# Optimization experiments

Hardware: AMD Instinct MI355X
Metric: run time of the kernel (lower is better)

## Reference

```python
import jax, jax.numpy as jnp
import numpy as np
import math

D_MODEL = 1024
NUM_HEADS = 16
HEAD_DIM = D_MODEL // NUM_HEADS
BLOCK_SIZE = 64
THRESHOLD = 0.99


def setup_inputs() -> dict:
    key = jax.random.key(0)
    ks = jax.random.split(key, 12)
    B, S, D = 2, 2048, D_MODEL
    scale = 1.0 / math.sqrt(D)
    x = jax.random.normal(ks[0], (B, S, D), dtype=jnp.float32)
    G_ii = jax.random.uniform(ks[1], (B, S), dtype=jnp.float32)
    # Linear weights stored as [in, out]; applied as x @ W + b (matches nn.Linear math).
    Wq = jax.random.normal(ks[2], (D, D), dtype=jnp.float32) * scale
    bq = jnp.zeros((D,), dtype=jnp.float32)
    Wk = jax.random.normal(ks[3], (D, D), dtype=jnp.float32) * scale
    bk = jnp.zeros((D,), dtype=jnp.float32)
    Wv = jax.random.normal(ks[4], (D, D), dtype=jnp.float32) * scale
    bv = jnp.zeros((D,), dtype=jnp.float32)
    Wo = jax.random.normal(ks[5], (D, D), dtype=jnp.float32) * scale
    bo = jnp.zeros((D,), dtype=jnp.float32)
    return {"x": x, "G_ii": G_ii, "Wq": Wq, "bq": bq, "Wk": Wk, "bk": bk,
            "Wv": Wv, "bv": bv, "Wo": Wo, "bo": bo}


def reference(x, G_ii, Wq, bq, Wk, bk, Wv, bv, Wo, bo):
    B, S, D = x.shape
    H, hd, bs = NUM_HEADS, HEAD_DIM, BLOCK_SIZE
    nb = S // bs

    # Projections and head split: [B, H, S, hd]
    q = (x @ Wq + bq).reshape(B, S, H, hd).transpose(0, 2, 1, 3)
    k = (x @ Wk + bk).reshape(B, S, H, hd).transpose(0, 2, 1, 3)
    v = (x @ Wv + bv).reshape(B, S, H, hd).transpose(0, 2, 1, 3)

    # Per-query-block scattering energy keep mask: block kept iff max |G_ii| >= threshold
    energy = jnp.abs(G_ii)                              # [B, S]
    block_max = energy.reshape(B, nb, bs).max(axis=-1)  # [B, nb]
    keep = (block_max >= THRESHOLD)                     # [B, nb] bool
    row_keep = jnp.repeat(keep, bs, axis=1)             # [B, S]

    # Kept query blocks attend densely (non-causal) over all keys; skipped blocks output zero.
    scores = jnp.einsum('bhqd,bhkd->bhqk', q, k) / math.sqrt(hd)  # [B, H, S, S]
    attn = jax.nn.softmax(scores, axis=-1)
    out = jnp.einsum('bhqk,bhkd->bhqd', attn, v)                  # [B, H, S, hd]
    out = out * row_keep[:, None, :, None].astype(out.dtype)

    out = out.transpose(0, 2, 1, 3).reshape(B, S, D)
    return out @ Wo + bo
```

## Files before the change

### kernel.cpp

```cpp
#include <hip/hip_runtime.h>
#include <math.h>

#define D_MODEL   1024
#define NUM_HEADS 16
#define HEAD_DIM  64
#define BS        64
#define NB        32
#define S_LEN     2048
#define BATCH     2
#define M_ROWS    (BATCH * S_LEN)
#define THRESH    0.99f
#define SCEXP     0.18033688f
#define NPH       (BATCH * NB * NUM_HEADS)
#define SPLITK    4

typedef __attribute__((ext_vector_type(8))) short bf16x8;
typedef __attribute__((ext_vector_type(8))) _Float16 f16x8;
typedef __attribute__((ext_vector_type(2))) __fp16 fp16v2;
typedef __attribute__((ext_vector_type(4))) float f32x4;

__device__ __forceinline__ unsigned short f2bf(float f) {
    unsigned int u = __float_as_uint(f);
    u += 0x7fff + ((u >> 16) & 1);
    return (unsigned short)(u >> 16);
}

__device__ __forceinline__ unsigned int pkrtz(float a, float b) {
    fp16v2 r = __builtin_amdgcn_cvt_pkrtz(a, b);
    return __builtin_bit_cast(unsigned int, r);
}

__device__ __forceinline__ void gload16(const void* gptr, void* lptr) {
    __builtin_amdgcn_global_load_lds(
        (const __attribute__((address_space(1))) void*)gptr,
        (__attribute__((address_space(3))) void*)lptr, 16, 0, 0);
}

__global__ __launch_bounds__(256) void prep_kernel(
    const float* __restrict__ x, const float* __restrict__ G,
    const float* __restrict__ Wq, const float* __restrict__ Wk,
    const float* __restrict__ Wv, const float* __restrict__ Wo,
    unsigned short* __restrict__ xb, unsigned short* __restrict__ wcat,
    unsigned short* __restrict__ wot, int* __restrict__ keep, int* __restrict__ work)
{
    const int bid = blockIdx.x, tid = threadIdx.x;
    __shared__ float T[64][65];

    if (bid < 2048) {
        size_t i = ((size_t)bid * 256 + tid) * 8;
        float4 a = *(const float4*)(x + i);
        float4 b = *(const float4*)(x + i + 4);
        uint4 o;
        o.x = (unsigned int)f2bf(a.x) | ((unsigned int)f2bf(a.y) << 16);
        o.y = (unsigned int)f2bf(a.z) | ((unsigned int)f2bf(a.w) << 16);
        o.z = (unsigned int)f2bf(b.x) | ((unsigned int)f2bf(b.y) << 16);
        o.w = (unsigned int)f2bf(b.z) | ((unsigned int)f2bf(b.w) << 16);
        *(uint4*)(xb + i) = o;
    } else if (bid < 3072) {
        int i = bid - 2048;
        int mat = i >> 8, rem = i & 255;
        int k0 = (rem & 15) * 64, n0 = (rem >> 4) * 64;
        const float* W = (mat == 0) ? Wq : (mat == 1) ? Wk : (mat == 2) ? Wv : Wo;
        int rr = tid >> 4, c4 = (tid & 15) * 4;
        #pragma unroll
        for (int j = 0; j < 4; j++) {
            int row = rr + j * 16;
            float4 v = *(const float4*)(W + (size_t)(k0 + row) * 1024 + n0 + c4);
            T[row][c4 + 0] = v.x; T[row][c4 + 1] = v.y;
            T[row][c4 + 2] = v.z; T[row][c4 + 3] = v.w;
        }
        __syncthreads();
        unsigned short* dst = (mat < 3) ? (wcat + (size_t)mat * 1024 * 1024) : wot;
        #pragma unroll
        for (int j = 0; j < 4; j++) {
            int n = rr + j * 16;
            unsigned int lo = (unsigned int)f2bf(T[c4 + 0][n]) | ((unsigned int)f2bf(T[c4 + 1][n]) << 16);
            unsigned int hi = (unsigned int)f2bf(T[c4 + 2][n]) | ((unsigned int)f2bf(T[c4 + 3][n]) << 16);
            *(uint2*)(dst + (size_t)(n0 + n) * 1024 + k0 + c4) = make_uint2(lo, hi);
        }
    } else {
        if (tid < 64) {
            int t = tid;
            const float4* g = (const float4*)(G + (size_t)t * 64);
            float mx = 0.f;
            #pragma unroll
            for (int j = 0; j < 16; j++) {
                float4 v = g[j];
                mx = fmaxf(mx, fmaxf(fmaxf(fabsf(v.x), fabsf(v.y)), fmaxf(fabsf(v.z), fabsf(v.w))));
            }
            bool k = (mx >= THRESH);
            unsigned long long bal = __ballot(k);
            int nk = __popcll(bal);
            unsigned long long below = bal & ((1ull << t) - 1ull);
            int nbelow = (int)__popcll(below);
            keep[t] = k ? 1 : 0;
            if (t == 0) work[0] = nk;
            int pos = k ? nbelow : (nk + t - nbelow);
            work[1 + pos] = t;
        }
    }
}

__global__ __launch_bounds__(256, 4) void gemm_qkv(
    const unsigned short* __restrict__ A, const unsigned short* __restrict__ Bt,
    const float* __restrict__ bq, const float* __restrict__ bk, const float* __restrict__ bv,
    const int* __restrict__ keep, unsigned short* __restrict__ qk, unsigned short* __restrict__ vt)
{
    const int n0 = blockIdx.x * 128, m0 = blockIdx.y * 64;
    const int tid = threadIdx.x, w = tid >> 6, lane = tid & 63;
    const int quad = lane >> 4, l16 = lane & 15;
    const int kindb = n0 >> 10;
    if (kindb == 0 && !keep[blockIdx.y]) return;

    __shared__ union {
        struct { unsigned short As[2][64 * 32]; unsigned short Bs[2][128 * 32]; } s;
        unsigned short qkr[64 * 136];
        unsigned short vr[128 * 72];
    } u;

    f32x4 acc[4][2];
    #pragma unroll
    for (int mt = 0; mt < 4; mt++)
        #pragma unroll
        for (int nt = 0; nt < 2; nt++) acc[mt][nt] = (f32x4){0.f, 0.f, 0.f, 0.f};

    #define QSTAGE(it_, p_)                                                             \
        {                                                                               \
            int k0_ = (it_) * 32;                                                       \
            { int s_ = w * 64 + lane; int row = s_ >> 2, cl = s_ & 3;                   \
              int c = cl ^ ((row >> 1) & 3);                                            \
              gload16(A + (size_t)(m0 + row) * 1024 + k0_ + c * 8,                      \
                      &u.s.As[p_][(w * 64) * 8]); }                                     \
            _Pragma("unroll")                                                           \
            for (int j = 0; j < 2; j++) {                                               \
                int s_ = w * 128 + j * 64 + lane; int row = s_ >> 2, cl = s_ & 3;       \
                int c = cl ^ ((row >> 1) & 3);                                          \
                gload16(Bt + (size_t)(n0 + row) * 1024 + k0_ + c * 8,                   \
                        &u.s.Bs[p_][(w * 128 + j * 64) * 8]);                           \
            }                                                                           \
        }

    QSTAGE(0, 0)

    for (int it = 0; it < 32; it++) {
        const int p = it & 1;
        __syncthreads();
        if (it + 1 < 32) QSTAGE(it + 1, (it + 1) & 1)

        bf16x8 af[4], bfr[2];
        #pragma unroll
        for (int mt = 0; mt < 4; mt++) {
            int row = mt * 16 + l16;
            int cl = quad ^ ((row >> 1) & 3);
            af[mt] = *(const bf16x8*)&u.s.As[p][(row * 4 + cl) * 8];
        }
        #pragma unroll
        for (int nt = 0; nt < 2; nt++) {
            int row = w * 32 + nt * 16 + l16;
            int cl = quad ^ ((row >> 1) & 3);
            bfr[nt] = *(const bf16x8*)&u.s.Bs[p][(row * 4 + cl) * 8];
        }
        #pragma unroll
        for (int mt = 0; mt < 4; mt++)
            #pragma unroll
            for (int nt = 0; nt < 2; nt++)
                acc[mt][nt] = __builtin_amdgcn_mfma_f32_16x16x32_bf16(af[mt], bfr[nt], acc[mt][nt], 0, 0, 0);
    }
    __syncthreads();

    if (kindb < 2) {
        const float* bp = (kindb == 0) ? bq : bk;
        const float sc = (kindb == 0) ? SCEXP : 1.0f;
        #pragma unroll
        for (int nt = 0; nt < 2; nt++) {
            int coll = w * 32 + nt * 16 + l16;
            float bb = bp[(n0 & 1023) + coll];
            #pragma unroll
            for (int mt = 0; mt < 4; mt++)
                #pragma unroll
                for (int r = 0; r < 4; r++) {
                    int row = mt * 16 + quad * 4 + r;
                    u.qkr[row * 136 + coll] = f2bf((acc[mt][nt][r] + bb) * sc);
                }
        }
        __syncthreads();
        #pragma unroll
        for (int i = 0; i < 4; i++) {
            int s_ = tid + i * 256;
            int row = s_ >> 4, c16 = s_ & 15;
            uint4 v = *(const uint4*)&u.qkr[row * 136 + c16 * 8];
            *(uint4*)(qk + (size_t)(m0 + row) * 2048 + n0 + c16 * 8) = v;
        }
    } else {
        #pragma unroll
        for (int nt = 0; nt < 2; nt++) {
            int coll = w * 32 + nt * 16 + l16;
            float bb = bv[(n0 - 2048) + coll];
            #pragma unroll
            for (int mt = 0; mt < 4; mt++) {
                int s0 = mt * 16 + quad * 4;
                uint2 pv;
                pv.x = pkrtz(acc[mt][nt][0] + bb, acc[mt][nt][1] + bb);
                pv.y = pkrtz(acc[mt][nt][2] + bb, acc[mt][nt][3] + bb);
                *(uint2*)&u.vr[coll * 72 + s0] = pv;
            }
        }
        __syncthreads();
        const int b_ = m0 >> 11, sbase = m0 & 2047;
        #pragma unroll
        for (int i = 0; i < 4; i++) {
            int s_ = tid + i * 256;
            int coll = s_ >> 3, ch = s_ & 7;
            uint4 v = *(const uint4*)&u.vr[coll * 72 + ch * 8];
            int colg = n0 - 2048 + coll;
            int h_ = colg >> 6, d = colg & 63;
            *(uint4*)(vt + ((size_t)(b_ * NUM_HEADS + h_) * HEAD_DIM + d) * 2048 + sbase + ch * 8) = v;
        }
    }
}

__global__ __launch_bounds__(256, 4) void gemm_out(
    const unsigned short* __restrict__ A, const unsigned short* __restrict__ Bt,
    const float* __restrict__ bo, const int* __restrict__ keep, float* __restrict__ out)
{
    const int n0 = blockIdx.x * 64, m0 = blockIdx.y * 64;
    const int tid = threadIdx.x, w = tid >> 6, lane = tid & 63;
    const int quad = lane >> 4, l16 = lane & 15;
    const int wm = w >> 1, wn = w & 1;

    if (!keep[blockIdx.y]) {
        #pragma unroll
        for (int i = 0; i < 4; i++) {
            int s_ = tid + i * 256;
            int row = s_ >> 4, c = (s_ & 15) * 4;
            *(float4*)(out + (size_t)(m0 + row) * 1024 + n0 + c) = *(const float4*)(bo + n0 + c);
        }
        return;
    }

    __shared__ unsigned short Asl[2][64 * 32];
    __shared__ unsigned short Bsl[2][64 * 32];

    f32x4 acc[2][2];
    #pragma unroll
    for (int mt = 0; mt < 2; mt++)
        #pragma unroll
        for (int nt = 0; nt < 2; nt++) acc[mt][nt] = (f32x4){0.f, 0.f, 0.f, 0.f};

    #define OSTAGE(it_, p_)                                                             \
        {                                                                               \
            int k0_ = (it_) * 32;                                                       \
            int s_ = w * 64 + lane; int row = s_ >> 2, cl = s_ & 3;                     \
            int c = cl ^ ((row >> 1) & 3);                                              \
            gload16(A  + (size_t)(m0 + row) * 1024 + k0_ + c * 8, &Asl[p_][(w * 64) * 8]); \
            gload16(Bt + (size_t)(n0 + row) * 1024 + k0_ + c * 8, &Bsl[p_][(w * 64) * 8]); \
        }

    OSTAGE(0, 0)

    for (int it = 0; it < 32; it++) {
        const int p = it & 1;
        __syncthreads();
        if (it + 1 < 32) OSTAGE(it + 1, (it + 1) & 1)

        bf16x8 af[2], bfr[2];
        #pragma unroll
        for (int mt = 0; mt < 2; mt++) {
            int row = wm * 32 + mt * 16 + l16;
            int cl = quad ^ ((row >> 1) & 3);
            af[mt] = *(const bf16x8*)&Asl[p][(row * 4 + cl) * 8];
        }
        #pragma unroll
        for (int nt = 0; nt < 2; nt++) {
            int row = wn * 32 + nt * 16 + l16;
            int cl = quad ^ ((row >> 1) & 3);
            bfr[nt] = *(const bf16x8*)&Bsl[p][(row * 4 + cl) * 8];
        }
        #pragma unroll
        for (int mt = 0; mt < 2; mt++)
            #pragma unroll
            for (int nt = 0; nt < 2; nt++)
                acc[mt][nt] = __builtin_amdgcn_mfma_f32_16x16x32_bf16(af[mt], bfr[nt], acc[mt][nt], 0, 0, 0);
    }

    #pragma unroll
    for (int nt = 0; nt < 2; nt++) {
        int col = n0 + wn * 32 + nt * 16 + l16;
        float bb = bo[col];
        #pragma unroll
        for (int mt = 0; mt < 2; mt++) {
            int mb = m0 + wm * 32 + mt * 16 + quad * 4;
            #pragma unroll
            for (int r = 0; r < 4; r++)
                out[(size_t)(mb + r) * 1024 + col] = acc[mt][nt][r] + bb;
        }
    }
}

__global__ __launch_bounds__(256, 4) void attn_kernel(
    const unsigned short* __restrict__ qk, const unsigned short* __restrict__ Vtg,
    const int* __restrict__ work,
    unsigned short* __restrict__ opart, float* __restrict__ lpart)
{
    const int bx = blockIdx.x, half = blockIdx.y;
    const int pair = bx >> 4, h = bx & 15;
    const int tid  = threadIdx.x;
    const int w    = tid >> 6, lane = tid & 63;
    const int quad = lane >> 4, l16 = lane & 15;

    if (pair >= work[0]) return;
    const int e = work[1 + pair];
    const int b = e >> 5, qblk = e & 31;

    __shared__ unsigned short Kbuf[BS * HEAD_DIM];
    __shared__ unsigned short Vbuf[HEAD_DIM * BS];
    __shared__ unsigned short Pt[4][16 * 64];

    const int KEYS = S_LEN / SPLITK;
    const int NCH  = KEYS / BS;
    const unsigned short* Qb = qk + (size_t)(b * S_LEN) * 2048 + h * 64;
    const unsigned short* Kb = qk + (size_t)(b * S_LEN + half * KEYS) * 2048 + 1024 + h * 64;
    const unsigned short* Vb = Vtg + (size_t)(b * NUM_HEADS + h) * HEAD_DIM * 2048 + half * KEYS;

    const int qrow = qblk * BS + w * 16 + l16;
    bf16x8 qf[2];
    #pragma unroll
    for (int ks = 0; ks < 2; ks++)
        qf[ks] = *(const bf16x8*)(Qb + (size_t)qrow * 2048 + ks * 32 + quad * 8);

    f32x4 o[4];
    #pragma unroll
    for (int mt = 0; mt < 4; mt++) o[mt] = (f32x4){0.f, 0.f, 0.f, 0.f};
    float l = 0.f;

    const int sA = w * 128 + lane, sB = sA + 64;
    const int rA = sA >> 3, cA = (sA & 7) ^ (rA & 7);
    const int rB = sB >> 3, cB = (sB & 7) ^ (rB & 7);
    const size_t koA = (size_t)rA * 2048 + cA * 8, koB = (size_t)rB * 2048 + cB * 8;

    uint4 kr0, kr1, vr0, vr1;
    #define LOADREGS(kc_)                                                       \
        {                                                                       \
            const unsigned short* kg_ = Kb + (size_t)(kc_) * BS * 2048;         \
            const unsigned short* vg_ = Vb + (size_t)(kc_) * BS;                \
            kr0 = *(const uint4*)(kg_ + koA); kr1 = *(const uint4*)(kg_ + koB); \
            vr0 = *(const uint4*)(vg_ + koA); vr1 = *(const uint4*)(vg_ + koB); \
        }
    #define WRITELDS()                                                          \
        {                                                                       \
            *(uint4*)&Kbuf[(size_t)sA * 8] = kr0;                               \
            *(uint4*)&Kbuf[(size_t)sB * 8] = kr1;                               \
            *(uint4*)&Vbuf[(size_t)sA * 8] = vr0;                               \
            *(uint4*)&Vbuf[(size_t)sB * 8] = vr1;                               \
        }

    LOADREGS(0)
    WRITELDS()
    __syncthreads();

    for (int kc = 0; kc < NCH; kc++) {
        if (kc + 1 < NCH) LOADREGS(kc + 1)

        f32x4 st[4];
        #pragma unroll
        for (int mt = 0; mt < 4; mt++) {
            f32x4 acc = {0.f, 0.f, 0.f, 0.f};
            #pragma unroll
            for (int ks = 0; ks < 2; ks++) {
                int kk = mt * 16 + l16;
                bf16x8 kf = *(const bf16x8*)&Kbuf[(size_t)(kk * 8 + ((ks * 4 + quad) ^ (kk & 7))) * 8];
                acc = __builtin_amdgcn_mfma_f32_16x16x32_bf16(kf, qf[ks], acc, 0, 0, 0);
            }
            st[mt] = acc;
        }

        float pv[16], sum = 0.f;
        #pragma unroll
        for (int mt = 0; mt < 4; mt++)
            #pragma unroll
            for (int r = 0; r < 4; r++) {
                float ex = exp2f(st[mt][r]);
                pv[mt * 4 + r] = ex; sum += ex;
            }
        sum += __shfl_xor(sum, 16, 64);
        sum += __shfl_xor(sum, 32, 64);
        l += sum;

        #pragma unroll
        for (int mt = 0; mt < 4; mt++) {
            unsigned int lo = pkrtz(pv[mt * 4 + 0], pv[mt * 4 + 1]);
            unsigned int hi = pkrtz(pv[mt * 4 + 2], pv[mt * 4 + 3]);
            int c16 = 2 * mt + (quad >> 1);
            *(uint2*)&Pt[w][l16 * 64 + ((c16 ^ (l16 & 7)) * 8 + (quad & 1) * 4)] = make_uint2(lo, hi);
        }

        #pragma unroll
        for (int ks = 0; ks < 2; ks++) {
            f16x8 pf = *(const f16x8*)&Pt[w][l16 * 64 + (((4 * ks + quad) ^ (l16 & 7)) * 8)];
            #pragma unroll
            for (int mt = 0; mt < 4; mt++) {
                int d = mt * 16 + l16;
                f16x8 vf = *(const f16x8*)&Vbuf[(size_t)(d * 8 + ((ks * 4 + quad) ^ (d & 7))) * 8];
                o[mt] = __builtin_amdgcn_mfma_f32_16x16x32_f16(vf, pf, o[mt], 0, 0, 0);
            }
        }

        __syncthreads();
        if (kc + 1 < NCH) {
            WRITELDS()
            __syncthreads();
        }
    }

    unsigned short* ob = opart + ((size_t)(half * NPH + bx)) * 4096 + tid * 16;
    uint4 w0, w1;
    w0.x = pkrtz(o[0][0], o[0][1]); w0.y = pkrtz(o[0][2], o[0][3]);
    w0.z = pkrtz(o[1][0], o[1][1]); w0.w = pkrtz(o[1][2], o[1][3]);
    w1.x = pkrtz(o[2][0], o[2][1]); w1.y = pkrtz(o[2][2], o[2][3]);
    w1.z = pkrtz(o[3][0], o[3][1]); w1.w = pkrtz(o[3][2], o[3][3]);
    *(uint4*)ob = w0;
    *(uint4*)(ob + 8) = w1;
    if (quad == 0) lpart[(size_t)(half * NPH + bx) * 64 + w * 16 + l16] = l;
}

__global__ __launch_bounds__(256) void attn_combine(
    const unsigned short* __restrict__ opart, const float* __restrict__ lpart,
    const int* __restrict__ work, unsigned short* __restrict__ attn_out)
{
    const int bx = blockIdx.x;
    const int pair = bx >> 4, h = bx & 15;
    const int tid  = threadIdx.x;
    const int w    = tid >> 6, lane = tid & 63;
    const int quad = lane >> 4, l16 = lane & 15;

    const int e = work[1 + pair];
    const int b = e >> 5, qblk = e & 31;
    unsigned short* ablk = attn_out + ((size_t)(b * S_LEN + qblk * BS)) * D_MODEL + h * HEAD_DIM;

    if (pair >= work[0]) {
        uint4 z = make_uint4(0, 0, 0, 0);
        #pragma unroll
        for (int i = 0; i < 2; i++) {
            int u = tid + i * 256;
            int row = u >> 3, c8 = (u & 7) * 8;
            *(uint4*)(ablk + (size_t)row * D_MODEL + c8) = z;
        }
        return;
    }

    __shared__ float Obuf[4][HEAD_DIM * 17];

    float osum[16];
    #pragma unroll
    for (int j = 0; j < 16; j++) osum[j] = 0.f;
    float lsum = 0.f;
    #pragma unroll
    for (int hf = 0; hf < SPLITK; hf++) {
        const f16x8* pp = (const f16x8*)(opart + ((size_t)hf * NPH + bx) * 4096 + tid * 16);
        f16x8 a0 = pp[0], a1 = pp[1];
        #pragma unroll
        for (int j = 0; j < 8; j++) {
            osum[j]     += (float)a0[j];
            osum[8 + j] += (float)a1[j];
        }
        lsum += lpart[((size_t)hf * NPH + bx) * 64 + w * 16 + l16];
    }
    float inv = 1.0f / lsum;

    #pragma unroll
    for (int mt = 0; mt < 4; mt++)
        #pragma unroll
        for (int r = 0; r < 4; r++)
            Obuf[w][(mt * 16 + quad * 4 + r) * 17 + l16] = osum[mt * 4 + r] * inv;
    #pragma unroll
    for (int i = 0; i < 4; i++) {
        int uu = lane + 64 * i;
        int row = uu >> 4, d4 = (uu & 15) * 4;
        float x0 = Obuf[w][(d4 + 0) * 17 + row];
        float x1 = Obuf[w][(d4 + 1) * 17 + row];
        float x2 = Obuf[w][(d4 + 2) * 17 + row];
        float x3 = Obuf[w][(d4 + 3) * 17 + row];
        unsigned int lo = (unsigned int)f2bf(x0) | ((unsigned int)f2bf(x1) << 16);
        unsigned int hi = (unsigned int)f2bf(x2) | ((unsigned int)f2bf(x3) << 16);
        *(uint2*)(ablk + (size_t)(w * 16 + row) * D_MODEL + d4) = make_uint2(lo, hi);
    }
}

extern "C" void kernel_launch(void* const* d_in, const int* in_sizes, int n_in,
                              void* d_out, int out_size, void* d_ws, size_t ws_size,
                              hipStream_t stream) {
    const float* x  = (const float*)d_in[0];
    const float* G  = (const float*)d_in[1];
    const float* Wq = (const float*)d_in[2];
    const float* bq = (const float*)d_in[3];
    const float* Wk = (const float*)d_in[4];
    const float* bk = (const float*)d_in[5];
    const float* Wv = (const float*)d_in[6];
    const float* bv = (const float*)d_in[7];
    const float* Wo = (const float*)d_in[8];
    const float* bo = (const float*)d_in[9];
    float* out = (float*)d_out;

    char* wsp = (char*)d_ws;
    int* keep = (int*)wsp;
    int* work = keep + 64;
    unsigned short* xb    = (unsigned short*)(wsp + 1024);
    unsigned short* wcat  = xb + (size_t)M_ROWS * D_MODEL;
    unsigned short* wot   = wcat + (size_t)3 * 1024 * 1024;
    unsigned short* qk    = wot + (size_t)1024 * 1024;
    unsigned short* vt    = qk + (size_t)M_ROWS * 2048;
    unsigned short* attnb = vt + (size_t)BATCH * NUM_HEADS * HEAD_DIM * 2048;
    unsigned short* opart = attnb + (size_t)M_ROWS * D_MODEL;
    float* lpart = (float*)(opart + (size_t)SPLITK * NPH * 4096);

    prep_kernel<<<3073, 256, 0, stream>>>(x, G, Wq, Wk, Wv, Wo, xb, wcat, wot, keep, work);

    gemm_qkv<<<dim3(3072 / 128, M_ROWS / 64), 256, 0, stream>>>(
        xb, wcat, bq, bk, bv, keep, qk, vt);

    attn_kernel<<<dim3(NPH, SPLITK), 256, 0, stream>>>(qk, vt, work, opart, lpart);
    attn_combine<<<NPH, 256, 0, stream>>>(opart, lpart, work, attnb);

    gemm_out<<<dim3(1024 / 64, M_ROWS / 64), 256, 0, stream>>>(attnb, wot, bo, keep, out);
}
```

Measured before the change: 191.8 us.

## Enlarge QKV GEMM tile to 128x128 with 2x2 warp layout

```diff
diff --git a/kernel.cpp b/kernel.cpp
--- a/kernel.cpp
+++ b/kernel.cpp
@@ -101,42 +101,44 @@
     }
 }
 
-__global__ __launch_bounds__(256, 4) void gemm_qkv(
+__global__ __launch_bounds__(256) void gemm_qkv(
     const unsigned short* __restrict__ A, const unsigned short* __restrict__ Bt,
     const float* __restrict__ bq, const float* __restrict__ bk, const float* __restrict__ bv,
     const int* __restrict__ keep, unsigned short* __restrict__ qk, unsigned short* __restrict__ vt)
 {
-    const int n0 = blockIdx.x * 128, m0 = blockIdx.y * 64;
+    const int n0 = blockIdx.x * 128, m0 = blockIdx.y * 128;
     const int tid = threadIdx.x, w = tid >> 6, lane = tid & 63;
     const int quad = lane >> 4, l16 = lane & 15;
+    const int wm = w >> 1, wn = w & 1;
     const int kindb = n0 >> 10;
-    if (kindb == 0 && !keep[blockIdx.y]) return;
+    const int kb0 = m0 >> 6;
+    const bool dropped = (!keep[kb0]) && (!keep[kb0 + 1]);
+    if (kindb == 0 && dropped) return;
 
     __shared__ union {
-        struct { unsigned short As[2][64 * 32]; unsigned short Bs[2][128 * 32]; } s;
+        struct { unsigned short As[2][128 * 32]; unsigned short Bs[2][128 * 32]; } s;
         unsigned short qkr[64 * 136];
         unsigned short vr[128 * 72];
     } u;
 
-    f32x4 acc[4][2];
+    f32x4 acc[4][4];
     #pragma unroll
     for (int mt = 0; mt < 4; mt++)
         #pragma unroll
-        for (int nt = 0; nt < 2; nt++) acc[mt][nt] = (f32x4){0.f, 0.f, 0.f, 0.f};
+        for (int nt = 0; nt < 4; nt++) acc[mt][nt] = (f32x4){0.f, 0.f, 0.f, 0.f};
 
     #define QSTAGE(it_, p_)                                                             \
         {                                                                               \
             int k0_ = (it_) * 32;                                                       \
-            { int s_ = w * 64 + lane; int row = s_ >> 2, cl = s_ & 3;                   \
-              int c = cl ^ ((row >> 1) & 3);                                            \
-              gload16(A + (size_t)(m0 + row) * 1024 + k0_ + c * 8,                      \
-                      &u.s.As[p_][(w * 64) * 8]); }                                     \
             _Pragma("unroll")                                                           \
             for (int j = 0; j < 2; j++) {                                               \
-                int s_ = w * 128 + j * 64 + lane; int row = s_ >> 2, cl = s_ & 3;       \
+                int s_ = w * 128 + j * 64 + lane;                                       \
+                int row = s_ >> 2, cl = s_ & 3;                                         \
                 int c = cl ^ ((row >> 1) & 3);                                          \
+                gload16(A  + (size_t)(m0 + row) * 1024 + k0_ + c * 8,                   \
+                        &u.s.As[p_][(size_t)(w * 128 + j * 64) * 8]);                   \
                 gload16(Bt + (size_t)(n0 + row) * 1024 + k0_ + c * 8,                   \
-                        &u.s.Bs[p_][(w * 128 + j * 64) * 8]);                           \
+                        &u.s.Bs[p_][(size_t)(w * 128 + j * 64) * 8]);                   \
             }                                                                           \
         }
 
@@ -147,23 +149,23 @@
         __syncthreads();
         if (it + 1 < 32) QSTAGE(it + 1, (it + 1) & 1)
 
-        bf16x8 af[4], bfr[2];
+        bf16x8 af[4], bfr[4];
         #pragma unroll
         for (int mt = 0; mt < 4; mt++) {
-            int row = mt * 16 + l16;
+            int row = wm * 64 + mt * 16 + l16;
             int cl = quad ^ ((row >> 1) & 3);
             af[mt] = *(const bf16x8*)&u.s.As[p][(row * 4 + cl) * 8];
         }
         #pragma unroll
-        for (int nt = 0; nt < 2; nt++) {
-            int row = w * 32 + nt * 16 + l16;
+        for (int nt = 0; nt < 4; nt++) {
+            int row = wn * 64 + nt * 16 + l16;
             int cl = quad ^ ((row >> 1) & 3);
             bfr[nt] = *(const bf16x8*)&u.s.Bs[p][(row * 4 + cl) * 8];
         }
         #pragma unroll
         for (int mt = 0; mt < 4; mt++)
             #pragma unroll
-            for (int nt = 0; nt < 2; nt++)
+            for (int nt = 0; nt < 4; nt++)
                 acc[mt][nt] = __builtin_amdgcn_mfma_f32_16x16x32_bf16(af[mt], bfr[nt], acc[mt][nt], 0, 0, 0);
     }
     __syncthreads();
@@ -172,49 +174,62 @@
         const float* bp = (kindb == 0) ? bq : bk;
         const float sc = (kindb == 0) ? SCEXP : 1.0f;
         #pragma unroll
-        for (int nt = 0; nt < 2; nt++) {
-            int coll = w * 32 + nt * 16 + l16;
-            float bb = bp[(n0 & 1023) + coll];
-            #pragma unroll
-            for (int mt = 0; mt < 4; mt++)
+        for (int pass = 0; pass < 2; pass++) {
+            if (wm == pass) {
                 #pragma unroll
-                for (int r = 0; r < 4; r++) {
-                    int row = mt * 16 + quad * 4 + r;
-                    u.qkr[row * 136 + coll] = f2bf((acc[mt][nt][r] + bb) * sc);
+                for (int nt = 0; nt < 4; nt++) {
+                    int coll = wn * 64 + nt * 16 + l16;
+                    float bb = bp[(n0 & 1023) + coll];
+                    #pragma unroll
+                    for (int mt = 0; mt < 4; mt++)
+                        #pragma unroll
+                        for (int r = 0; r < 4; r++) {
+                            int rl = mt * 16 + quad * 4 + r;
+                            u.qkr[rl * 136 + coll] = f2bf((acc[mt][nt][r] + bb) * sc);
+                        }
                 }
-        }
-        __syncthreads();
-        #pragma unroll
-        for (int i = 0; i < 4; i++) {
-            int s_ = tid + i * 256;
-            int row = s_ >> 4, c16 = s_ & 15;
-            uint4 v = *(const uint4*)&u.qkr[row * 136 + c16 * 8];
-            *(uint4*)(qk + (size_t)(m0 + row) * 2048 + n0 + c16 * 8) = v;
+            }
+            __syncthreads();
+            #pragma unroll
+            for (int i = 0; i < 4; i++) {
+                int s_ = tid + i * 256;
+                int row = s_ >> 4, c16 = s_ & 15;
+                uint4 v = *(const uint4*)&u.qkr[row * 136 + c16 * 8];
+                *(uint4*)(qk + (size_t)(m0 + pass * 64 + row) * 2048 + n0 + c16 * 8) = v;
+            }
+            if (pass == 0) __syncthreads();
         }
     } else {
-        #pragma unroll
-        for (int nt = 0; nt < 2; nt++) {
-            int coll = w * 32 + nt * 16 + l16;
-            float bb = bv[(n0 - 2048) + coll];
-            #pragma unroll
-            for (int mt = 0; mt < 4; mt++) {
-                int s0 = mt * 16 + quad * 4;
-                uint2 pv;
-                pv.x = pkrtz(acc[mt][nt][0] + bb, acc[mt][nt][1] + bb);
-                pv.y = pkrtz(acc[mt][nt][2] + bb, acc[mt][nt][3] + bb);
-                *(uint2*)&u.vr[coll * 72 + s0] = pv;
-            }
-        }
-        __syncthreads();
-        const int b_ = m0 >> 11, sbase = m0 & 2047;
-        #pragma unroll
-        for (int i = 0; i < 4; i++) {
-            int s_ = tid + i * 256;
-            int coll = s_ >> 3, ch = s_ & 7;
-            uint4 v = *(const uint4*)&u.vr[coll * 72 + ch * 8];
-            int colg = n0 - 2048 + coll;
-            int h_ = colg >> 6, d = colg & 63;
-            *(uint4*)(vt + ((size_t)(b_ * NUM_HEADS + h_) * HEAD_DIM + d) * 2048 + sbase + ch * 8) = v;
+        const int b_ = m0 >> 11, sb = m0 & 2047;
+        #pragma unroll
+        for (int pass = 0; pass < 2; pass++) {
+            if (wm == pass) {
+                #pragma unroll
+                for (int nt = 0; nt < 4; nt++) {
+                    int coll = wn * 64 + nt * 16 + l16;
+                    float bb = bv[(n0 - 2048) + coll];
+                    #pragma unroll
+                    for (int mt = 0; mt < 4; mt++) {
+                        int s0 = mt * 16 + quad * 4;
+                        uint2 pv;
+                        pv.x = pkrtz(acc[mt][nt][0] + bb, acc[mt][nt][1] + bb);
+                        pv.y = pkrtz(acc[mt][nt][2] + bb, acc[mt][nt][3] + bb);
+                        *(uint2*)&u.vr[coll * 72 + s0] = pv;
+                    }
+                }
+            }
+            __syncthreads();
+            #pragma unroll
+            for (int i = 0; i < 4; i++) {
+                int s_ = tid + i * 256;
+                int coll = s_ >> 3, ch = s_ & 7;
+                uint4 v = *(const uint4*)&u.vr[coll * 72 + ch * 8];
+                int colg = n0 - 2048 + coll;
+                int h_ = colg >> 6, d = colg & 63;
+                *(uint4*)(vt + ((size_t)(b_ * NUM_HEADS + h_) * HEAD_DIM + d) * 2048 +
+                          sb + pass * 64 + ch * 8) = v;
+            }
+            if (pass == 0) __syncthreads();
         }
     }
 }
@@ -515,7 +530,7 @@
 
     prep_kernel<<<3073, 256, 0, stream>>>(x, G, Wq, Wk, Wv, Wo, xb, wcat, wot, keep, work);
 
-    gemm_qkv<<<dim3(3072 / 128, M_ROWS / 64), 256, 0, stream>>>(
+    gemm_qkv<<<dim3(3072 / 128, M_ROWS / 128), 256, 0, stream>>>(
         xb, wcat, bq, bk, bv, keep, qk, vt);
 
     attn_kernel<<<dim3(NPH, SPLITK), 256, 0, stream>>>(qk, vt, work, opart, lpart);
```

Result: slower. 197.0 us (+2.7%).
